# Kernel optimization log

Measured on AMD Instinct MI355X. Metric: run time of the kernel, lower is better.

Reference implementation:

```python
import jax, jax.numpy as jnp
import numpy as np

N = 100000   # nodes
E = 1600000  # edges
IN = 128     # input feature dim
HID = 64     # hidden = IN // 2
OUT = 8      # output_size
B = 16384    # lookup batch


def sage_conv(x, src, dst, W_l, W_r, b, n):
    # PyG SAGEConv (aggr='mean', root_weight=True):
    # out = lin_l(mean_{j in N(i)} x_j) + lin_r(x_i)
    msgs = x[src]                                              # [E, F] gather
    agg = jax.ops.segment_sum(msgs, dst, num_segments=n)       # [N, F] scatter-add
    deg = jax.ops.segment_sum(jnp.ones((src.shape[0],), x.dtype), dst, num_segments=n)
    mean = agg / jnp.maximum(deg, 1.0)[:, None]                # zero-degree -> 0
    return mean @ W_l + x @ W_r + b


def setup_inputs() -> dict:
    key = jax.random.key(0)
    ks = jax.random.split(key, 10)
    node_feats = jax.random.normal(ks[0], (N, IN), dtype=jnp.float32)
    edge_index = jax.random.randint(ks[1], (2, E), 0, N, dtype=jnp.int64)
    idx = jax.random.randint(ks[2], (B,), 0, N, dtype=jnp.int64)
    dropout_mask = jax.random.uniform(ks[3], (N, HID), dtype=jnp.float32)
    s1 = 1.0 / np.sqrt(IN)
    s2 = 1.0 / np.sqrt(HID)
    W1_l = jax.random.normal(ks[4], (IN, HID), dtype=jnp.float32) * s1
    W1_r = jax.random.normal(ks[5], (IN, HID), dtype=jnp.float32) * s1
    b1 = jnp.zeros((HID,), dtype=jnp.float32)
    W2_l = jax.random.normal(ks[6], (HID, OUT), dtype=jnp.float32) * s2
    W2_r = jax.random.normal(ks[7], (HID, OUT), dtype=jnp.float32) * s2
    b2 = jnp.zeros((OUT,), dtype=jnp.float32)
    return {"node_feats": node_feats, "edge_index": edge_index, "idx": idx,
            "dropout_mask": dropout_mask, "W1_l": W1_l, "W1_r": W1_r, "b1": b1,
            "W2_l": W2_l, "W2_r": W2_r, "b2": b2}


def reference(node_feats, edge_index, idx, dropout_mask, W1_l, W1_r, b1, W2_l, W2_r, b2):
    n = node_feats.shape[0]
    src, dst = edge_index[0], edge_index[1]
    h = sage_conv(node_feats, src, dst, W1_l, W1_r, b1, n)     # [N, HID]
    h = jax.nn.relu(h)
    keep = (dropout_mask > 0.5).astype(h.dtype)                # F.dropout p=0.5
    h = h * keep * 2.0                                         # inverted dropout scale 1/(1-p)
    emb = sage_conv(h, src, dst, W2_l, W2_r, b2, n)            # [N, OUT]
    return emb[idx]                                            # [B, OUT]
```

## Files before the change

### kernel.cpp

```cpp
#include <hip/hip_runtime.h>
#include <hip/hip_fp16.h>

#define IN_F 128
#define HID_F 64
#define OUT_F 8

#define BSHIFT 8
#define BGRAN 256
#define BCAP 6144
#define CHUNK 4096
#define EPT (CHUNK / 256)

#if defined(__has_builtin)
#if __has_builtin(__builtin_amdgcn_fdot2)
#define HAS_FDOT2 1
#endif
#endif

typedef _Float16 h2v __attribute__((ext_vector_type(2)));

__global__ __launch_bounds__(512) void init_bcur(int* __restrict__ bcur) {
  bcur[threadIdx.x] = (int)threadIdx.x * BCAP;
}

__global__ __launch_bounds__(256) void bucket_scatter(
    const int* __restrict__ src, const int* __restrict__ dst,
    int* __restrict__ bcur, int2* __restrict__ ebuf, int n_edges) {
  __shared__ int hist[512];
  __shared__ int base[512];
  int t = threadIdx.x;
  for (int i = t; i < 512; i += 256) hist[i] = 0;
  __syncthreads();
  int e0 = blockIdx.x * CHUNK;
  int2 ed[EPT];
  int bk[EPT];
#pragma unroll
  for (int k = 0; k < EPT; ++k) {
    int e = e0 + k * 256 + t;
    if (e < n_edges) {
      ed[k].x = src[e];
      ed[k].y = dst[e];
      bk[k] = ed[k].y >> BSHIFT;
      atomicAdd(&hist[bk[k]], 1);
    } else {
      bk[k] = -1;
    }
  }
  __syncthreads();
  for (int i = t; i < 512; i += 256) {
    int c = hist[i];
    base[i] = c ? atomicAdd(&bcur[i], c) : 0;
  }
  __syncthreads();
  for (int i = t; i < 512; i += 256) hist[i] = 0;
  __syncthreads();
#pragma unroll
  for (int k = 0; k < EPT; ++k) {
    if (bk[k] >= 0) {
      int r = atomicAdd(&hist[bk[k]], 1);
      ebuf[base[bk[k]] + r] = ed[k];
    }
  }
}

__global__ __launch_bounds__(256) void deg_kernel(
    const int2* __restrict__ ebuf, const int* __restrict__ bcur,
    int* __restrict__ deg_i, int n_nodes) {
  __shared__ int hist[BGRAN];
  int b = blockIdx.x;
  int t = threadIdx.x;
  hist[t] = 0;
  __syncthreads();
  int beg = b * BCAP;
  int cnt = bcur[b] - beg;
  for (int j = t; j < cnt; j += 256)
    atomicAdd(&hist[ebuf[beg + j].y & (BGRAN - 1)], 1);
  __syncthreads();
  int node = b * BGRAN + t;
  if (node < n_nodes) deg_i[node] = hist[t];
}

__global__ __launch_bounds__(256) void scan_local(
    const int* __restrict__ deg_i, int* __restrict__ offs_l,
    int* __restrict__ blk_sums, int n) {
  __shared__ int tsum[256];
  int t = threadIdx.x;
  int i0 = blockIdx.x * 1024 + t * 4;
  int v0 = 0, v1 = 0, v2 = 0, v3 = 0;
  if (i0 + 3 < n) {
    int4 d = *(const int4*)(deg_i + i0);
    v0 = d.x; v1 = d.y; v2 = d.z; v3 = d.w;
  } else {
    if (i0 + 0 < n) v0 = deg_i[i0 + 0];
    if (i0 + 1 < n) v1 = deg_i[i0 + 1];
    if (i0 + 2 < n) v2 = deg_i[i0 + 2];
    if (i0 + 3 < n) v3 = deg_i[i0 + 3];
  }
  tsum[t] = v0 + v1 + v2 + v3;
  __syncthreads();
  for (int d = 1; d < 256; d <<= 1) {
    int x = 0;
    if (t >= d) x = tsum[t - d];
    __syncthreads();
    if (t >= d) tsum[t] += x;
    __syncthreads();
  }
  if (t == 255) blk_sums[blockIdx.x] = tsum[255];
  int run = (t == 0) ? 0 : tsum[t - 1];
  int o0 = run, o1 = o0 + v0, o2 = o1 + v1, o3 = o2 + v2;
  if (i0 + 3 < n) {
    *(int4*)(offs_l + i0) = make_int4(o0, o1, o2, o3);
  } else {
    if (i0 + 0 < n) offs_l[i0 + 0] = o0;
    if (i0 + 1 < n) offs_l[i0 + 1] = o1;
    if (i0 + 2 < n) offs_l[i0 + 2] = o2;
    if (i0 + 3 < n) offs_l[i0 + 3] = o3;
  }
}

__global__ __launch_bounds__(256) void scan_blk(
    int* __restrict__ blk_sums, int nblk) {
  __shared__ int s[256];
  int t = threadIdx.x;
  s[t] = (t < nblk) ? blk_sums[t] : 0;
  __syncthreads();
  for (int d = 1; d < 256; d <<= 1) {
    int x = 0;
    if (t >= d) x = s[t - d];
    __syncthreads();
    if (t >= d) s[t] += x;
    __syncthreads();
  }
  if (t < nblk) blk_sums[t] = (t == 0) ? 0 : s[t - 1];
}

__global__ __launch_bounds__(256) void csr_scatter(
    const int2* __restrict__ ebuf, const int* __restrict__ bcur,
    const int* __restrict__ offs_l, const int* __restrict__ blk_sums,
    int* __restrict__ offs_f, int* __restrict__ csr_src, int n_nodes) {
  __shared__ int cur[BGRAN];
  int b = blockIdx.x;
  int t = threadIdx.x;
  int node = b * BGRAN + t;
  int base = blk_sums[b >> 2];
  if (node < n_nodes) {
    int o = offs_l[node] + base;
    offs_f[node] = o;
    cur[t] = o;
  } else {
    cur[t] = 0;
  }
  __syncthreads();
  int beg = b * BCAP;
  int cnt = bcur[b] - beg;
  for (int j = t; j < cnt; j += 256) {
    int2 e = ebuf[beg + j];
    int p = atomicAdd(&cur[e.y & (BGRAN - 1)], 1);
    csr_src[p] = e.x;
  }
}

#define BM 128
#define BK 32
__global__ __launch_bounds__(256, 4) void k1_proj(
    const float* __restrict__ x,
    const float* __restrict__ Wl,
    const float* __restrict__ Wr,
    const float* __restrict__ b1,
    __half* __restrict__ y1h,
    float* __restrict__ r1,
    int n_nodes) {
  __shared__ h2v XS2[BK / 2][BM];
  __shared__ h2v WS2[BK / 2][128];
  int tid = threadIdx.x;
  int tx = tid & 15;
  int ty = tid >> 4;
  int n0 = blockIdx.x * BM;

  float acc[8][8];
#pragma unroll
  for (int i = 0; i < 8; ++i)
#pragma unroll
    for (int j = 0; j < 8; ++j) acc[i][j] = 0.f;

  for (int kb = 0; kb < IN_F; kb += BK) {
    {
      int nn0 = tid >> 3;
      int k4 = (tid & 7) * 4;
      int kp0 = (tid & 7) * 2;
#pragma unroll
      for (int p = 0; p < 4; ++p) {
        int nn = nn0 + p * 32;
        int gs = min(n0 + nn, n_nodes - 1);
        float4 v = *(const float4*)(x + (size_t)gs * IN_F + kb + k4);
        XS2[kp0][nn] = h2v{(_Float16)v.x, (_Float16)v.y};
        XS2[kp0 + 1][nn] = h2v{(_Float16)v.z, (_Float16)v.w};
      }
    }
    {
#pragma unroll
      for (int p = 0; p < 2; ++p) {
        int s = tid + p * 256;
        int kp = s >> 5;
        int col = (s & 31) * 4;
        int k0 = kb + kp * 2;
        const float* pa = (col < 64) ? (Wl + (size_t)k0 * HID_F + col)
                                     : (Wr + (size_t)k0 * HID_F + (col - 64));
        const float* pb = (col < 64) ? (Wl + (size_t)(k0 + 1) * HID_F + col)
                                     : (Wr + (size_t)(k0 + 1) * HID_F + (col - 64));
        float4 wa = *(const float4*)pa;
        float4 wb = *(const float4*)pb;
        WS2[kp][col + 0] = h2v{(_Float16)wa.x, (_Float16)wb.x};
        WS2[kp][col + 1] = h2v{(_Float16)wa.y, (_Float16)wb.y};
        WS2[kp][col + 2] = h2v{(_Float16)wa.z, (_Float16)wb.z};
        WS2[kp][col + 3] = h2v{(_Float16)wa.w, (_Float16)wb.w};
      }
    }
    __syncthreads();
#pragma unroll 4
    for (int kp = 0; kp < BK / 2; ++kp) {
      h2v xv[8], wv[8];
#pragma unroll
      for (int i = 0; i < 8; ++i) xv[i] = XS2[kp][ty * 8 + i];
#pragma unroll
      for (int j = 0; j < 8; ++j) wv[j] = WS2[kp][tx * 8 + j];
#pragma unroll
      for (int i = 0; i < 8; ++i)
#pragma unroll
        for (int j = 0; j < 8; ++j) {
#ifdef HAS_FDOT2
          acc[i][j] = __builtin_amdgcn_fdot2(xv[i], wv[j], acc[i][j], false);
#else
          acc[i][j] += (float)xv[i][0] * (float)wv[j][0] +
                       (float)xv[i][1] * (float)wv[j][1];
#endif
        }
    }
    __syncthreads();
  }

  int outb = tx * 8;
  bool isR = (outb >= HID_F);
  int ob = isR ? outb - HID_F : outb;
  if (isR) {
    float bb[8];
#pragma unroll
    for (int j = 0; j < 8; ++j) bb[j] = b1[ob + j];
#pragma unroll
    for (int i = 0; i < 8; ++i) {
      int node = n0 + ty * 8 + i;
      if (node < n_nodes) {
        float4 o0 = make_float4(acc[i][0] + bb[0], acc[i][1] + bb[1],
                                acc[i][2] + bb[2], acc[i][3] + bb[3]);
        float4 o1 = make_float4(acc[i][4] + bb[4], acc[i][5] + bb[5],
                                acc[i][6] + bb[6], acc[i][7] + bb[7]);
        *(float4*)(r1 + (size_t)node * HID_F + ob) = o0;
        *(float4*)(r1 + (size_t)node * HID_F + ob + 4) = o1;
      }
    }
  } else {
#pragma unroll
    for (int i = 0; i < 8; ++i) {
      int node = n0 + ty * 8 + i;
      if (node < n_nodes) {
        __half hh[8];
#pragma unroll
        for (int j = 0; j < 8; ++j) hh[j] = __float2half(acc[i][j]);
        *(uint4*)(y1h + (size_t)node * HID_F + ob) = *(uint4*)hh;
      }
    }
  }
}

__global__ __launch_bounds__(256) void agg1_fused(
    const __half* __restrict__ y1h,
    const float* __restrict__ r1,
    const int* __restrict__ deg_i,
    const int* __restrict__ offs,
    const int* __restrict__ csr_src,
    const float* __restrict__ mask,
    float* __restrict__ h,
    int n_nodes) {
  int node = (blockIdx.x * blockDim.x + threadIdx.x) >> 6;
  int lane = threadIdx.x & 63;
  if (node >= n_nodes) return;
  int q = lane >> 4;
  int f4 = lane & 15;
  int beg = offs[node];
  int d = deg_i[node];
  const int* cp = csr_src + beg;
  float a0 = 0.f, a1 = 0.f, a2 = 0.f, a3 = 0.f;
  int j = 0;
  for (; j + 16 <= d; j += 16) {
    int s0 = cp[j + q];
    int s1 = cp[j + 4 + q];
    int s2 = cp[j + 8 + q];
    int s3 = cp[j + 12 + q];
    uint2 g0 = *(const uint2*)(y1h + (size_t)s0 * HID_F + f4 * 4);
    uint2 g1 = *(const uint2*)(y1h + (size_t)s1 * HID_F + f4 * 4);
    uint2 g2 = *(const uint2*)(y1h + (size_t)s2 * HID_F + f4 * 4);
    uint2 g3 = *(const uint2*)(y1h + (size_t)s3 * HID_F + f4 * 4);
    float2 p0 = __half22float2(*(const __half2*)&g0.x);
    float2 p1 = __half22float2(*(const __half2*)&g0.y);
    float2 p2 = __half22float2(*(const __half2*)&g1.x);
    float2 p3 = __half22float2(*(const __half2*)&g1.y);
    float2 p4 = __half22float2(*(const __half2*)&g2.x);
    float2 p5 = __half22float2(*(const __half2*)&g2.y);
    float2 p6 = __half22float2(*(const __half2*)&g3.x);
    float2 p7 = __half22float2(*(const __half2*)&g3.y);
    a0 += (p0.x + p2.x) + (p4.x + p6.x);
    a1 += (p0.y + p2.y) + (p4.y + p6.y);
    a2 += (p1.x + p3.x) + (p5.x + p7.x);
    a3 += (p1.y + p3.y) + (p5.y + p7.y);
  }
  for (; j < d; j += 4) {
    int e = j + q;
    if (e < d) {
      int s = cp[e];
      uint2 g = *(const uint2*)(y1h + (size_t)s * HID_F + f4 * 4);
      float2 p0 = __half22float2(*(const __half2*)&g.x);
      float2 p1 = __half22float2(*(const __half2*)&g.y);
      a0 += p0.x; a1 += p0.y; a2 += p1.x; a3 += p1.y;
    }
  }
  a0 += __shfl_xor(a0, 16); a0 += __shfl_xor(a0, 32);
  a1 += __shfl_xor(a1, 16); a1 += __shfl_xor(a1, 32);
  a2 += __shfl_xor(a2, 16); a2 += __shfl_xor(a2, 32);
  a3 += __shfl_xor(a3, 16); a3 += __shfl_xor(a3, 32);
  if (q == 0) {
    float inv = 1.0f / fmaxf((float)d, 1.0f);
    size_t o = (size_t)node * HID_F + f4 * 4;
    float4 rr = *(const float4*)(r1 + o);
    float4 mm = *(const float4*)(mask + o);
    float vx = fmaxf(a0 * inv + rr.x, 0.f);
    float vy = fmaxf(a1 * inv + rr.y, 0.f);
    float vz = fmaxf(a2 * inv + rr.z, 0.f);
    float vw = fmaxf(a3 * inv + rr.w, 0.f);
    vx = (mm.x > 0.5f) ? vx * 2.f : 0.f;
    vy = (mm.y > 0.5f) ? vy * 2.f : 0.f;
    vz = (mm.z > 0.5f) ? vz * 2.f : 0.f;
    vw = (mm.w > 0.5f) ? vw * 2.f : 0.f;
    *(float4*)(h + o) = make_float4(vx, vy, vz, vw);
  }
}

__global__ __launch_bounds__(256) void k3b_z(
    const float* __restrict__ h,
    const float* __restrict__ W2l,
    __half* __restrict__ z,
    int n_nodes) {
  __shared__ float WS[HID_F][OUT_F];
  int tid = threadIdx.x;
  if (tid < 128) {
    float4 w = *(const float4*)(W2l + tid * 4);
    *(float4*)&WS[tid >> 1][(tid & 1) * 4] = w;
  }
  __syncthreads();
  int node = blockIdx.x * blockDim.x + tid;
  if (node >= n_nodes) return;
  const float* hr = h + (size_t)node * HID_F;
  float acc[8] = {0, 0, 0, 0, 0, 0, 0, 0};
  for (int k = 0; k < HID_F; k += 4) {
    float4 hv = *(const float4*)(hr + k);
    float hh[4] = {hv.x, hv.y, hv.z, hv.w};
#pragma unroll
    for (int j = 0; j < 4; ++j) {
      float4 w0 = *(const float4*)&WS[k + j][0];
      float4 w1 = *(const float4*)&WS[k + j][4];
      acc[0] += hh[j] * w0.x; acc[1] += hh[j] * w0.y;
      acc[2] += hh[j] * w0.z; acc[3] += hh[j] * w0.w;
      acc[4] += hh[j] * w1.x; acc[5] += hh[j] * w1.y;
      acc[6] += hh[j] * w1.z; acc[7] += hh[j] * w1.w;
    }
  }
  __half hz[8];
#pragma unroll
  for (int j = 0; j < 8; ++j) hz[j] = __float2half(acc[j]);
  *(uint4*)(z + (size_t)node * OUT_F) = *(uint4*)hz;
}

__global__ __launch_bounds__(256) void out_fused(
    const int* __restrict__ idx,
    const __half* __restrict__ z,
    const int* __restrict__ deg_i,
    const int* __restrict__ offs,
    const int* __restrict__ csr_src,
    const float* __restrict__ h,
    const float* __restrict__ W2r,
    const float* __restrict__ b2,
    float* __restrict__ out,
    int n_batch) {
  int b = (blockIdx.x * blockDim.x + threadIdx.x) >> 6;
  int lane = threadIdx.x & 63;
  if (b >= n_batch) return;
  int i = idx[b];
  int e8 = lane >> 3;
  int o = lane & 7;
  int beg = offs[i];
  int d = deg_i[i];
  float acc = 0.f;
  for (int j = e8; j < d; j += 8) {
    int s = csr_src[beg + j];
    acc += __half2float(z[(size_t)s * OUT_F + o]);
  }
  float dv = fmaxf((float)d, 1.0f);
  float v = acc / dv;
  const float* hr = h + (size_t)i * HID_F;
#pragma unroll
  for (int jj = 0; jj < 8; ++jj) {
    int k = e8 * 8 + jj;
    v += hr[k] * W2r[k * OUT_F + o];
  }
  v += __shfl_xor(v, 8);
  v += __shfl_xor(v, 16);
  v += __shfl_xor(v, 32);
  if (e8 == 0) out[(size_t)b * OUT_F + o] = v + b2[o];
}

extern "C" void kernel_launch(void* const* d_in, const int* in_sizes, int n_in,
                              void* d_out, int out_size, void* d_ws, size_t ws_size,
                              hipStream_t stream) {
  const float* x    = (const float*)d_in[0];
  const int*   ei   = (const int*)d_in[1];
  const int*   idx  = (const int*)d_in[2];
  const float* mask = (const float*)d_in[3];
  const float* W1l  = (const float*)d_in[4];
  const float* W1r  = (const float*)d_in[5];
  const float* b1   = (const float*)d_in[6];
  const float* W2l  = (const float*)d_in[7];
  const float* W2r  = (const float*)d_in[8];
  const float* b2   = (const float*)d_in[9];
  float* out = (float*)d_out;

  int n_nodes = in_sizes[0] / IN_F;
  int n_edges = in_sizes[1] / 2;
  int n_batch = in_sizes[2];
  const int* src = ei;
  const int* dst = ei + n_edges;

  int nbuk = (n_nodes + BGRAN - 1) / BGRAN;
  int nchunk = (n_edges + CHUNK - 1) / CHUNK;
  int nblk = (n_nodes + 1023) / 1024;

  char* ws = (char*)d_ws;
  size_t off = 0;
  size_t y1_bytes = (size_t)n_nodes * HID_F * sizeof(__half);
  size_t eb_bytes = (size_t)nbuk * BCAP * sizeof(int2);
  size_t regA = (y1_bytes > eb_bytes) ? y1_bytes : eb_bytes;
  __half* y1h = (__half*)(ws + off);
  int2* ebuf  = (int2*)(ws + off); off += regA;
  float* r1 = (float*)(ws + off); off += (size_t)n_nodes * HID_F * 4;
  float* h  = (float*)(ws + off); off += (size_t)n_nodes * HID_F * 4;
  __half* z = (__half*)(ws + off); off += (size_t)n_nodes * OUT_F * sizeof(__half);
  int* deg_i  = (int*)(ws + off); off += (size_t)n_nodes * 4;
  int* offs_l = (int*)(ws + off); off += (size_t)n_nodes * 4;
  int* offs_f = (int*)(ws + off); off += (size_t)n_nodes * 4;
  int* csr_src = (int*)(ws + off); off += (size_t)n_edges * 4;
  int* blk_sums = (int*)(ws + off); off += 256 * 4;
  int* bcur     = (int*)(ws + off); off += 512 * 4;

  init_bcur<<<1, 512, 0, stream>>>(bcur);
  bucket_scatter<<<nchunk, 256, 0, stream>>>(src, dst, bcur, ebuf, n_edges);
  deg_kernel<<<nbuk, 256, 0, stream>>>(ebuf, bcur, deg_i, n_nodes);
  scan_local<<<nblk, 256, 0, stream>>>(deg_i, offs_l, blk_sums, n_nodes);
  scan_blk<<<1, 256, 0, stream>>>(blk_sums, nblk);
  csr_scatter<<<nbuk, 256, 0, stream>>>(ebuf, bcur, offs_l, blk_sums, offs_f, csr_src, n_nodes);

  k1_proj<<<(n_nodes + BM - 1) / BM, 256, 0, stream>>>(x, W1l, W1r, b1, y1h, r1, n_nodes);
  {
    long long th = (long long)n_nodes * HID_F;
    agg1_fused<<<(int)((th + 255) / 256), 256, 0, stream>>>(
        y1h, r1, deg_i, offs_f, csr_src, mask, h, n_nodes);
  }

  k3b_z<<<(n_nodes + 255) / 256, 256, 0, stream>>>(h, W2l, z, n_nodes);
  {
    long long th = (long long)n_batch * 64;
    out_fused<<<(int)((th + 255) / 256), 256, 0, stream>>>(idx, z, deg_i, offs_f, csr_src, h, W2r, b2, out, n_batch);
  }
}
```

Measured before the change: 279.0 us.

## Pack edges, build padded per-bucket CSR in one kernel, store intermediates in fp16

Measured after the change: 267.2 us. -4.2%, faster.

```diff
diff --git a/kernel.cpp b/kernel.cpp
--- a/kernel.cpp
+++ b/kernel.cpp
@@ -5,11 +5,13 @@
 #define HID_F 64
 #define OUT_F 8
 
-#define BSHIFT 8
-#define BGRAN 256
-#define BCAP 6144
+#define BSHIFT 7
+#define BGRAN 128
+#define BCAP 2688
+#define NBUK_MAX 784
 #define CHUNK 4096
 #define EPT (CHUNK / 256)
+#define CEPT ((BCAP + 255) / 256)
 
 #if defined(__has_builtin)
 #if __has_builtin(__builtin_amdgcn_fdot2)
@@ -19,145 +21,100 @@
 
 typedef _Float16 h2v __attribute__((ext_vector_type(2)));
 
-__global__ __launch_bounds__(512) void init_bcur(int* __restrict__ bcur) {
-  bcur[threadIdx.x] = (int)threadIdx.x * BCAP;
+__global__ __launch_bounds__(1024) void init_bcur(int* __restrict__ bcur, int nbuk) {
+  int t = threadIdx.x;
+  if (t < nbuk) bcur[t] = t * BCAP;
 }
 
 __global__ __launch_bounds__(256) void bucket_scatter(
     const int* __restrict__ src, const int* __restrict__ dst,
-    int* __restrict__ bcur, int2* __restrict__ ebuf, int n_edges) {
-  __shared__ int hist[512];
-  __shared__ int base[512];
+    int* __restrict__ bcur, int* __restrict__ ebuf, int n_edges) {
+  __shared__ int hist[NBUK_MAX];
+  __shared__ int base[NBUK_MAX];
   int t = threadIdx.x;
-  for (int i = t; i < 512; i += 256) hist[i] = 0;
+  for (int i = t; i < NBUK_MAX; i += 256) hist[i] = 0;
   __syncthreads();
   int e0 = blockIdx.x * CHUNK;
-  int2 ed[EPT];
+  int pk[EPT];
   int bk[EPT];
 #pragma unroll
   for (int k = 0; k < EPT; ++k) {
     int e = e0 + k * 256 + t;
     if (e < n_edges) {
-      ed[k].x = src[e];
-      ed[k].y = dst[e];
-      bk[k] = ed[k].y >> BSHIFT;
+      int s = src[e];
+      int d = dst[e];
+      bk[k] = d >> BSHIFT;
+      pk[k] = ((d & (BGRAN - 1)) << 24) | s;
       atomicAdd(&hist[bk[k]], 1);
     } else {
       bk[k] = -1;
     }
   }
   __syncthreads();
-  for (int i = t; i < 512; i += 256) {
+  for (int i = t; i < NBUK_MAX; i += 256) {
     int c = hist[i];
     base[i] = c ? atomicAdd(&bcur[i], c) : 0;
   }
   __syncthreads();
-  for (int i = t; i < 512; i += 256) hist[i] = 0;
+  for (int i = t; i < NBUK_MAX; i += 256) hist[i] = 0;
   __syncthreads();
 #pragma unroll
   for (int k = 0; k < EPT; ++k) {
     if (bk[k] >= 0) {
       int r = atomicAdd(&hist[bk[k]], 1);
-      ebuf[base[bk[k]] + r] = ed[k];
-    }
-  }
-}
-
-__global__ __launch_bounds__(256) void deg_kernel(
-    const int2* __restrict__ ebuf, const int* __restrict__ bcur,
-    int* __restrict__ deg_i, int n_nodes) {
+      ebuf[base[bk[k]] + r] = pk[k];
+    }
+  }
+}
+
+__global__ __launch_bounds__(256) void bucket_csr(
+    const int* __restrict__ ebuf, const int* __restrict__ bcur,
+    int* __restrict__ offs_f, int* __restrict__ deg_i,
+    int* __restrict__ csr_src, int n_nodes) {
   __shared__ int hist[BGRAN];
+  __shared__ int cur[BGRAN];
+  __shared__ int s[BGRAN];
+  __shared__ int lds_src[BCAP];
   int b = blockIdx.x;
   int t = threadIdx.x;
-  hist[t] = 0;
+  if (t < BGRAN) hist[t] = 0;
   __syncthreads();
   int beg = b * BCAP;
   int cnt = bcur[b] - beg;
-  for (int j = t; j < cnt; j += 256)
-    atomicAdd(&hist[ebuf[beg + j].y & (BGRAN - 1)], 1);
-  __syncthreads();
-  int node = b * BGRAN + t;
-  if (node < n_nodes) deg_i[node] = hist[t];
-}
-
-__global__ __launch_bounds__(256) void scan_local(
-    const int* __restrict__ deg_i, int* __restrict__ offs_l,
-    int* __restrict__ blk_sums, int n) {
-  __shared__ int tsum[256];
-  int t = threadIdx.x;
-  int i0 = blockIdx.x * 1024 + t * 4;
-  int v0 = 0, v1 = 0, v2 = 0, v3 = 0;
-  if (i0 + 3 < n) {
-    int4 d = *(const int4*)(deg_i + i0);
-    v0 = d.x; v1 = d.y; v2 = d.z; v3 = d.w;
-  } else {
-    if (i0 + 0 < n) v0 = deg_i[i0 + 0];
-    if (i0 + 1 < n) v1 = deg_i[i0 + 1];
-    if (i0 + 2 < n) v2 = deg_i[i0 + 2];
-    if (i0 + 3 < n) v3 = deg_i[i0 + 3];
-  }
-  tsum[t] = v0 + v1 + v2 + v3;
-  __syncthreads();
-  for (int d = 1; d < 256; d <<= 1) {
-    int x = 0;
-    if (t >= d) x = tsum[t - d];
+  int pk[CEPT];
+  int np = 0;
+  for (int j = t; j < cnt; j += 256) {
+    pk[np] = ebuf[beg + j];
+    atomicAdd(&hist[(unsigned)pk[np] >> 24], 1);
+    ++np;
+  }
+  __syncthreads();
+  if (t < BGRAN) s[t] = hist[t];
+  __syncthreads();
+  for (int d = 1; d < BGRAN; d <<= 1) {
+    int v = 0;
+    if (t >= d && t < BGRAN) v = s[t - d];
     __syncthreads();
-    if (t >= d) tsum[t] += x;
+    if (t >= d && t < BGRAN) s[t] += v;
     __syncthreads();
   }
-  if (t == 255) blk_sums[blockIdx.x] = tsum[255];
-  int run = (t == 0) ? 0 : tsum[t - 1];
-  int o0 = run, o1 = o0 + v0, o2 = o1 + v1, o3 = o2 + v2;
-  if (i0 + 3 < n) {
-    *(int4*)(offs_l + i0) = make_int4(o0, o1, o2, o3);
-  } else {
-    if (i0 + 0 < n) offs_l[i0 + 0] = o0;
-    if (i0 + 1 < n) offs_l[i0 + 1] = o1;
-    if (i0 + 2 < n) offs_l[i0 + 2] = o2;
-    if (i0 + 3 < n) offs_l[i0 + 3] = o3;
-  }
-}
-
-__global__ __launch_bounds__(256) void scan_blk(
-    int* __restrict__ blk_sums, int nblk) {
-  __shared__ int s[256];
-  int t = threadIdx.x;
-  s[t] = (t < nblk) ? blk_sums[t] : 0;
-  __syncthreads();
-  for (int d = 1; d < 256; d <<= 1) {
-    int x = 0;
-    if (t >= d) x = s[t - d];
-    __syncthreads();
-    if (t >= d) s[t] += x;
-    __syncthreads();
-  }
-  if (t < nblk) blk_sums[t] = (t == 0) ? 0 : s[t - 1];
-}
-
-__global__ __launch_bounds__(256) void csr_scatter(
-    const int2* __restrict__ ebuf, const int* __restrict__ bcur,
-    const int* __restrict__ offs_l, const int* __restrict__ blk_sums,
-    int* __restrict__ offs_f, int* __restrict__ csr_src, int n_nodes) {
-  __shared__ int cur[BGRAN];
-  int b = blockIdx.x;
-  int t = threadIdx.x;
-  int node = b * BGRAN + t;
-  int base = blk_sums[b >> 2];
-  if (node < n_nodes) {
-    int o = offs_l[node] + base;
-    offs_f[node] = o;
-    cur[t] = o;
-  } else {
-    cur[t] = 0;
-  }
-  __syncthreads();
-  int beg = b * BCAP;
-  int cnt = bcur[b] - beg;
-  for (int j = t; j < cnt; j += 256) {
-    int2 e = ebuf[beg + j];
-    int p = atomicAdd(&cur[e.y & (BGRAN - 1)], 1);
-    csr_src[p] = e.x;
-  }
+  if (t < BGRAN) {
+    int excl = (t == 0) ? 0 : s[t - 1];
+    cur[t] = excl;
+    int node = b * BGRAN + t;
+    if (node < n_nodes) {
+      offs_f[node] = beg + excl;
+      deg_i[node] = hist[t];
+    }
+  }
+  __syncthreads();
+  for (int i = 0; i < np; ++i) {
+    int dl = (unsigned)pk[i] >> 24;
+    int p = atomicAdd(&cur[dl], 1);
+    lds_src[p] = pk[i] & 0xFFFFFF;
+  }
+  __syncthreads();
+  for (int j = t; j < cnt; j += 256) csr_src[beg + j] = lds_src[j];
 }
 
 #define BM 128
@@ -167,8 +124,10 @@
     const float* __restrict__ Wl,
     const float* __restrict__ Wr,
     const float* __restrict__ b1,
+    const float* __restrict__ mask,
     __half* __restrict__ y1h,
-    float* __restrict__ r1,
+    __half* __restrict__ r1h,
+    unsigned long long* __restrict__ mbits,
     int n_nodes) {
   __shared__ h2v XS2[BK / 2][BM];
   __shared__ h2v WS2[BK / 2][128];
@@ -177,6 +136,19 @@
   int ty = tid >> 4;
   int n0 = blockIdx.x * BM;
 
+  {
+    int w = tid >> 6;
+    int lane = tid & 63;
+    for (int i = w; i < BM; i += 4) {
+      int node = n0 + i;
+      if (node < n_nodes) {
+        float mv = mask[(size_t)node * HID_F + lane];
+        unsigned long long bits = __ballot(mv > 0.5f);
+        if (lane == 0) mbits[node] = bits;
+      }
+    }
+  }
+
   float acc[8][8];
 #pragma unroll
   for (int i = 0; i < 8; ++i)
@@ -200,9 +172,9 @@
     {
 #pragma unroll
       for (int p = 0; p < 2; ++p) {
-        int s = tid + p * 256;
-        int kp = s >> 5;
-        int col = (s & 31) * 4;
+        int sidx = tid + p * 256;
+        int kp = sidx >> 5;
+        int col = (sidx & 31) * 4;
         int k0 = kb + kp * 2;
         const float* pa = (col < 64) ? (Wl + (size_t)k0 * HID_F + col)
                                      : (Wr + (size_t)k0 * HID_F + (col - 64));
@@ -242,44 +214,30 @@
   int outb = tx * 8;
   bool isR = (outb >= HID_F);
   int ob = isR ? outb - HID_F : outb;
-  if (isR) {
-    float bb[8];
-#pragma unroll
-    for (int j = 0; j < 8; ++j) bb[j] = b1[ob + j];
-#pragma unroll
-    for (int i = 0; i < 8; ++i) {
-      int node = n0 + ty * 8 + i;
-      if (node < n_nodes) {
-        float4 o0 = make_float4(acc[i][0] + bb[0], acc[i][1] + bb[1],
-                                acc[i][2] + bb[2], acc[i][3] + bb[3]);
-        float4 o1 = make_float4(acc[i][4] + bb[4], acc[i][5] + bb[5],
-                                acc[i][6] + bb[6], acc[i][7] + bb[7]);
-        *(float4*)(r1 + (size_t)node * HID_F + ob) = o0;
-        *(float4*)(r1 + (size_t)node * HID_F + ob + 4) = o1;
-      }
-    }
-  } else {
-#pragma unroll
-    for (int i = 0; i < 8; ++i) {
-      int node = n0 + ty * 8 + i;
-      if (node < n_nodes) {
-        __half hh[8];
-#pragma unroll
-        for (int j = 0; j < 8; ++j) hh[j] = __float2half(acc[i][j]);
-        *(uint4*)(y1h + (size_t)node * HID_F + ob) = *(uint4*)hh;
-      }
+  __half* dbuf = isR ? r1h : y1h;
+  float bb[8];
+#pragma unroll
+  for (int j = 0; j < 8; ++j) bb[j] = isR ? b1[ob + j] : 0.f;
+#pragma unroll
+  for (int i = 0; i < 8; ++i) {
+    int node = n0 + ty * 8 + i;
+    if (node < n_nodes) {
+      __half hh[8];
+#pragma unroll
+      for (int j = 0; j < 8; ++j) hh[j] = __float2half(acc[i][j] + bb[j]);
+      *(uint4*)(dbuf + (size_t)node * HID_F + ob) = *(uint4*)hh;
     }
   }
 }
 
 __global__ __launch_bounds__(256) void agg1_fused(
     const __half* __restrict__ y1h,
-    const float* __restrict__ r1,
+    const __half* __restrict__ r1h,
     const int* __restrict__ deg_i,
     const int* __restrict__ offs,
     const int* __restrict__ csr_src,
-    const float* __restrict__ mask,
-    float* __restrict__ h,
+    const unsigned long long* __restrict__ mbits,
+    __half* __restrict__ h_h,
     int n_nodes) {
   int node = (blockIdx.x * blockDim.x + threadIdx.x) >> 6;
   int lane = threadIdx.x & 63;
@@ -330,22 +288,27 @@
   if (q == 0) {
     float inv = 1.0f / fmaxf((float)d, 1.0f);
     size_t o = (size_t)node * HID_F + f4 * 4;
-    float4 rr = *(const float4*)(r1 + o);
-    float4 mm = *(const float4*)(mask + o);
-    float vx = fmaxf(a0 * inv + rr.x, 0.f);
-    float vy = fmaxf(a1 * inv + rr.y, 0.f);
-    float vz = fmaxf(a2 * inv + rr.z, 0.f);
-    float vw = fmaxf(a3 * inv + rr.w, 0.f);
-    vx = (mm.x > 0.5f) ? vx * 2.f : 0.f;
-    vy = (mm.y > 0.5f) ? vy * 2.f : 0.f;
-    vz = (mm.z > 0.5f) ? vz * 2.f : 0.f;
-    vw = (mm.w > 0.5f) ? vw * 2.f : 0.f;
-    *(float4*)(h + o) = make_float4(vx, vy, vz, vw);
+    uint2 rg = *(const uint2*)(r1h + o);
+    float2 r01 = __half22float2(*(const __half2*)&rg.x);
+    float2 r23 = __half22float2(*(const __half2*)&rg.y);
+    unsigned long long mb = mbits[node];
+    float vx = fmaxf(a0 * inv + r01.x, 0.f);
+    float vy = fmaxf(a1 * inv + r01.y, 0.f);
+    float vz = fmaxf(a2 * inv + r23.x, 0.f);
+    float vw = fmaxf(a3 * inv + r23.y, 0.f);
+    int fb = f4 * 4;
+    vx = ((mb >> (fb + 0)) & 1ull) ? vx * 2.f : 0.f;
+    vy = ((mb >> (fb + 1)) & 1ull) ? vy * 2.f : 0.f;
+    vz = ((mb >> (fb + 2)) & 1ull) ? vz * 2.f : 0.f;
+    vw = ((mb >> (fb + 3)) & 1ull) ? vw * 2.f : 0.f;
+    __half hh[4] = {__float2half(vx), __float2half(vy),
+                    __float2half(vz), __float2half(vw)};
+    *(uint2*)(h_h + o) = *(uint2*)hh;
   }
 }
 
 __global__ __launch_bounds__(256) void k3b_z(
-    const float* __restrict__ h,
+    const __half* __restrict__ h_h,
     const float* __restrict__ W2l,
     __half* __restrict__ z,
     int n_nodes) {
@@ -358,13 +321,17 @@
   __syncthreads();
   int node = blockIdx.x * blockDim.x + tid;
   if (node >= n_nodes) return;
-  const float* hr = h + (size_t)node * HID_F;
+  const __half* hr = h_h + (size_t)node * HID_F;
   float acc[8] = {0, 0, 0, 0, 0, 0, 0, 0};
-  for (int k = 0; k < HID_F; k += 4) {
-    float4 hv = *(const float4*)(hr + k);
-    float hh[4] = {hv.x, hv.y, hv.z, hv.w};
-#pragma unroll
-    for (int j = 0; j < 4; ++j) {
+  for (int k = 0; k < HID_F; k += 8) {
+    uint4 hv = *(const uint4*)(hr + k);
+    float2 f0 = __half22float2(*(const __half2*)&hv.x);
+    float2 f1 = __half22float2(*(const __half2*)&hv.y);
+    float2 f2 = __half22float2(*(const __half2*)&hv.z);
+    float2 f3 = __half22float2(*(const __half2*)&hv.w);
+    float hh[8] = {f0.x, f0.y, f1.x, f1.y, f2.x, f2.y, f3.x, f3.y};
+#pragma unroll
+    for (int j = 0; j < 8; ++j) {
       float4 w0 = *(const float4*)&WS[k + j][0];
       float4 w1 = *(const float4*)&WS[k + j][4];
       acc[0] += hh[j] * w0.x; acc[1] += hh[j] * w0.y;
@@ -385,7 +352,7 @@
     const int* __restrict__ deg_i,
     const int* __restrict__ offs,
     const int* __restrict__ csr_src,
-    const float* __restrict__ h,
+    const __half* __restrict__ h_h,
     const float* __restrict__ W2r,
     const float* __restrict__ b2,
     float* __restrict__ out,
@@ -405,11 +372,16 @@
   }
   float dv = fmaxf((float)d, 1.0f);
   float v = acc / dv;
-  const float* hr = h + (size_t)i * HID_F;
+  uint4 hv = *(const uint4*)(h_h + (size_t)i * HID_F + e8 * 8);
+  float2 f0 = __half22float2(*(const __half2*)&hv.x);
+  float2 f1 = __half22float2(*(const __half2*)&hv.y);
+  float2 f2 = __half22float2(*(const __half2*)&hv.z);
+  float2 f3 = __half22float2(*(const __half2*)&hv.w);
+  float hh[8] = {f0.x, f0.y, f1.x, f1.y, f2.x, f2.y, f3.x, f3.y};
 #pragma unroll
   for (int jj = 0; jj < 8; ++jj) {
     int k = e8 * 8 + jj;
-    v += hr[k] * W2r[k * OUT_F + o];
+    v += hh[jj] * W2r[k * OUT_F + o];
   }
   v += __shfl_xor(v, 8);
   v += __shfl_xor(v, 16);
@@ -440,42 +412,36 @@
 
   int nbuk = (n_nodes + BGRAN - 1) / BGRAN;
   int nchunk = (n_edges + CHUNK - 1) / CHUNK;
-  int nblk = (n_nodes + 1023) / 1024;
 
   char* ws = (char*)d_ws;
   size_t off = 0;
-  size_t y1_bytes = (size_t)n_nodes * HID_F * sizeof(__half);
-  size_t eb_bytes = (size_t)nbuk * BCAP * sizeof(int2);
-  size_t regA = (y1_bytes > eb_bytes) ? y1_bytes : eb_bytes;
-  __half* y1h = (__half*)(ws + off);
-  int2* ebuf  = (int2*)(ws + off); off += regA;
-  float* r1 = (float*)(ws + off); off += (size_t)n_nodes * HID_F * 4;
-  float* h  = (float*)(ws + off); off += (size_t)n_nodes * HID_F * 4;
-  __half* z = (__half*)(ws + off); off += (size_t)n_nodes * OUT_F * sizeof(__half);
-  int* deg_i  = (int*)(ws + off); off += (size_t)n_nodes * 4;
-  int* offs_l = (int*)(ws + off); off += (size_t)n_nodes * 4;
-  int* offs_f = (int*)(ws + off); off += (size_t)n_nodes * 4;
-  int* csr_src = (int*)(ws + off); off += (size_t)n_edges * 4;
-  int* blk_sums = (int*)(ws + off); off += 256 * 4;
-  int* bcur     = (int*)(ws + off); off += 512 * 4;
-
-  init_bcur<<<1, 512, 0, stream>>>(bcur);
+  __half* y1h = (__half*)(ws + off); off += (size_t)n_nodes * HID_F * 2;
+  __half* r1h = (__half*)(ws + off); off += (size_t)n_nodes * HID_F * 2;
+  __half* h_h = (__half*)(ws + off); off += (size_t)n_nodes * HID_F * 2;
+  __half* z   = (__half*)(ws + off); off += (size_t)n_nodes * OUT_F * 2;
+  unsigned long long* mbits = (unsigned long long*)(ws + off); off += (size_t)n_nodes * 8;
+  int* ebuf    = (int*)(ws + off); off += (size_t)nbuk * BCAP * 4;
+  int* csr_src = (int*)(ws + off); off += (size_t)nbuk * BCAP * 4;
+  int* deg_i   = (int*)(ws + off); off += (size_t)n_nodes * 4;
+  int* offs_f  = (int*)(ws + off); off += (size_t)n_nodes * 4;
+  int* bcur    = (int*)(ws + off); off += NBUK_MAX * 4;
+
+  init_bcur<<<1, 1024, 0, stream>>>(bcur, nbuk);
   bucket_scatter<<<nchunk, 256, 0, stream>>>(src, dst, bcur, ebuf, n_edges);
-  deg_kernel<<<nbuk, 256, 0, stream>>>(ebuf, bcur, deg_i, n_nodes);
-  scan_local<<<nblk, 256, 0, stream>>>(deg_i, offs_l, blk_sums, n_nodes);
-  scan_blk<<<1, 256, 0, stream>>>(blk_sums, nblk);
-  csr_scatter<<<nbuk, 256, 0, stream>>>(ebuf, bcur, offs_l, blk_sums, offs_f, csr_src, n_nodes);
-
-  k1_proj<<<(n_nodes + BM - 1) / BM, 256, 0, stream>>>(x, W1l, W1r, b1, y1h, r1, n_nodes);
+  k1_proj<<<(n_nodes + BM - 1) / BM, 256, 0, stream>>>(
+      x, W1l, W1r, b1, mask, y1h, r1h, mbits, n_nodes);
+  bucket_csr<<<nbuk, 256, 0, stream>>>(ebuf, bcur, offs_f, deg_i, csr_src, n_nodes);
+
   {
     long long th = (long long)n_nodes * HID_F;
     agg1_fused<<<(int)((th + 255) / 256), 256, 0, stream>>>(
-        y1h, r1, deg_i, offs_f, csr_src, mask, h, n_nodes);
-  }
-
-  k3b_z<<<(n_nodes + 255) / 256, 256, 0, stream>>>(h, W2l, z, n_nodes);
+        y1h, r1h, deg_i, offs_f, csr_src, mbits, h_h, n_nodes);
+  }
+
+  k3b_z<<<(n_nodes + 255) / 256, 256, 0, stream>>>(h_h, W2l, z, n_nodes);
   {
     long long th = (long long)n_batch * 64;
-    out_fused<<<(int)((th + 255) / 256), 256, 0, stream>>>(idx, z, deg_i, offs_f, csr_src, h, W2r, b2, out, n_batch);
-  }
-}
+    out_fused<<<(int)((th + 255) / 256), 256, 0, stream>>>(
+        idx, z, deg_i, offs_f, csr_src, h_h, W2r, b2, out, n_batch);
+  }
+}
```
